# Optimization experiments

Measured on AMD Instinct MI355X. Metric: run time of the kernel, lower is better.

Reference implementation:

```python
import jax, jax.numpy as jnp
import numpy as np

D_MODEL = 512
NUM_HEADS = 8
DEPTH = D_MODEL // NUM_HEADS
B, S = 8, 1024


def setup_inputs() -> dict:
    key = jax.random.key(0)
    ks = jax.random.split(key, 14)
    scale = 1.0 / np.sqrt(D_MODEL)
    inp = {
        "q_in": jax.random.normal(ks[0], (B, S, D_MODEL), jnp.float32),
        "k_in": jax.random.normal(ks[1], (B, S, D_MODEL), jnp.float32),
        "v_in": jax.random.normal(ks[2], (B, S, D_MODEL), jnp.float32),
        # padding mask: 1 = masked-out position
        "mask": jax.random.randint(ks[3], (B, 1, 1, S), 0, 2).astype(jnp.float32),
        "additional_weights": jax.random.uniform(ks[4], (B, S, S), jnp.float32),
        "wq": jax.random.normal(ks[5], (D_MODEL, D_MODEL), jnp.float32) * scale,
        "bq": jnp.zeros((D_MODEL,), jnp.float32),
        "wk": jax.random.normal(ks[6], (D_MODEL, D_MODEL), jnp.float32) * scale,
        "bk": jnp.zeros((D_MODEL,), jnp.float32),
        "wv": jax.random.normal(ks[7], (D_MODEL, D_MODEL), jnp.float32) * scale,
        "bv": jnp.zeros((D_MODEL,), jnp.float32),
        "wo": jax.random.normal(ks[8], (D_MODEL, D_MODEL), jnp.float32) * scale,
        "bo": jnp.zeros((D_MODEL,), jnp.float32),
    }
    return inp


def _split_heads(x):
    # [B, S, d_model] -> [B, H, S, depth]
    b, s, _ = x.shape
    return x.reshape(b, s, NUM_HEADS, DEPTH).transpose(0, 2, 1, 3)


def reference(q_in, k_in, v_in, mask, additional_weights,
              wq, bq, wk, bk, wv, bv, wo, bo):
    q = _split_heads(q_in @ wq + bq)  # [B,H,S,D]
    k = _split_heads(k_in @ wk + bk)
    v = _split_heads(v_in @ wv + bv)

    scores = jnp.einsum("bhqd,bhkd->bhqk", q, k) / jnp.sqrt(
        jnp.asarray(DEPTH, q.dtype))
    scores = scores + mask * -1e9
    attn = jax.nn.softmax(scores, axis=-1)
    # post-softmax multiplicative weights, broadcast over heads
    attn = attn * additional_weights[:, None, :, :]
    x = jnp.einsum("bhqk,bhkd->bhqd", attn, v)
    x = x.transpose(0, 2, 1, 3).reshape(q_in.shape[0], -1, D_MODEL)
    out = x @ wo + bo
    return out, attn
```

## Files before the change

### kernel.cpp

```cpp
#include <hip/hip_runtime.h>
#include <stdint.h>

typedef unsigned short u16;
typedef short bf16x8 __attribute__((ext_vector_type(8)));
typedef short bf16x4 __attribute__((ext_vector_type(4)));
typedef float f32x4 __attribute__((ext_vector_type(4)));
typedef u16 u16x8 __attribute__((ext_vector_type(8)));
typedef u16 u16x4 __attribute__((ext_vector_type(4)));

#define NHEADS 8
#define SEQ 1024
#define DM 512
#define DEPTH 64
#define BATCH 8

__device__ __forceinline__ u16 f2bf(float f) {
    union { float f; unsigned u; } v; v.f = f;
    unsigned r = v.u + 0x7FFF + ((v.u >> 16) & 1);
    return (u16)(r >> 16);
}

__device__ __forceinline__ f32x4 mfma_16x16x16_bf16(bf16x4 a, bf16x4 b, f32x4 c) {
#if __has_builtin(__builtin_amdgcn_mfma_f32_16x16x16bf16_1k)
    return __builtin_amdgcn_mfma_f32_16x16x16bf16_1k(a, b, c, 0, 0, 0);
#else
    asm("v_mfma_f32_16x16x16_bf16 %0, %1, %2, %0" : "+v"(c) : "v"(a), "v"(b));
    return c;
#endif
}

__global__ void __launch_bounds__(256) transpose512(
    const float* __restrict__ w0, const float* __restrict__ w1,
    const float* __restrict__ w2, const float* __restrict__ w3,
    u16* __restrict__ wt)
{
    __shared__ float tile[32][33];
    const float* w = (blockIdx.z == 0) ? w0 : (blockIdx.z == 1) ? w1
                   : (blockIdx.z == 2) ? w2 : w3;
    u16* o = wt + (size_t)blockIdx.z * (DM * DM);
    int rb = blockIdx.y * 32, cb = blockIdx.x * 32;
    int tx = threadIdx.x, ty = threadIdx.y;
    #pragma unroll
    for (int k = 0; k < 32; k += 8)
        tile[ty + k][tx] = w[(size_t)(rb + ty + k) * DM + cb + tx];
    __syncthreads();
    #pragma unroll
    for (int k = 0; k < 32; k += 8)
        o[(size_t)(cb + ty + k) * DM + rb + tx] = f2bf(tile[tx][ty + k]);
}

__global__ void __launch_bounds__(256) conv_bf16(
    const float* __restrict__ q, const float* __restrict__ k,
    const float* __restrict__ v,
    u16* __restrict__ oq, u16* __restrict__ ok, u16* __restrict__ ov)
{
    const float* src = (blockIdx.z == 0) ? q : (blockIdx.z == 1) ? k : v;
    u16* dst = (blockIdx.z == 0) ? oq : (blockIdx.z == 1) ? ok : ov;
    size_t i = ((size_t)blockIdx.x * 256 + threadIdx.x) * 8;
    f32x4 a = *(const f32x4*)(src + i);
    f32x4 b = *(const f32x4*)(src + i + 4);
    u16x8 o;
    #pragma unroll
    for (int j = 0; j < 4; j++) { o[j] = f2bf(a[j]); o[j + 4] = f2bf(b[j]); }
    *(u16x8*)(dst + i) = o;
}

template <int LAYOUT>
__device__ __forceinline__ void gemm_tile(
    const u16* __restrict__ A, const u16* __restrict__ wt,
    const float* __restrict__ bias, void* __restrict__ out_)
{
    const int tid = threadIdx.x;
    const int wid = tid >> 6, lane = tid & 63;
    const int wm = wid >> 1, wn = wid & 1;
    const int mb = blockIdx.y * 128 + wm * 64;
    const int nb = blockIdx.x * 128 + wn * 64;
    const int lr = lane & 15, g = lane >> 4, lk = g * 8;

    f32x4 acc[4][4];
    #pragma unroll
    for (int i = 0; i < 4; i++)
        #pragma unroll
        for (int j = 0; j < 4; j++) acc[i][j] = (f32x4)0.f;

    for (int ks = 0; ks < DM; ks += 32) {
        bf16x8 a[4], bf[4];
        #pragma unroll
        for (int mt = 0; mt < 4; mt++)
            a[mt] = *(const bf16x8*)(A + (size_t)(mb + mt * 16 + lr) * DM + ks + lk);
        #pragma unroll
        for (int nt = 0; nt < 4; nt++)
            bf[nt] = *(const bf16x8*)(wt + (size_t)(nb + nt * 16 + lr) * DM + ks + lk);
        #pragma unroll
        for (int mt = 0; mt < 4; mt++)
            #pragma unroll
            for (int nt = 0; nt < 4; nt++) {
                if (LAYOUT == 1)
                    acc[mt][nt] = __builtin_amdgcn_mfma_f32_16x16x32_bf16(
                        bf[nt], a[mt], acc[mt][nt], 0, 0, 0);
                else
                    acc[mt][nt] = __builtin_amdgcn_mfma_f32_16x16x32_bf16(
                        a[mt], bf[nt], acc[mt][nt], 0, 0, 0);
            }
    }

    #pragma unroll
    for (int mt = 0; mt < 4; mt++) {
        #pragma unroll
        for (int nt = 0; nt < 4; nt++) {
            #pragma unroll
            for (int r = 0; r < 4; r++) {
                if (LAYOUT == 1) {
                    int m = mb + mt * 16 + lr;
                    int n = nb + nt * 16 + 4 * g + r;
                    float val = acc[mt][nt][r] + bias[n];
                    int b_ = m >> 10, s = m & 1023, h = n >> 6, d = n & 63;
                    ((u16*)out_)[((size_t)((b_ * NHEADS + h) << 6) + d) * SEQ + s] = f2bf(val);
                } else {
                    int n = nb + nt * 16 + lr;
                    int m = mb + mt * 16 + 4 * g + r;
                    float val = acc[mt][nt][r] + bias[n];
                    if (LAYOUT == 2) {
                        ((float*)out_)[(size_t)m * DM + n] = val;
                    } else {
                        int b_ = m >> 10, s = m & 1023, h = n >> 6, d = n & 63;
                        ((u16*)out_)[(((size_t)(b_ * NHEADS + h) * SEQ + s) << 6) + d] = f2bf(val);
                    }
                }
            }
        }
    }
}

__global__ void __launch_bounds__(256) qkv_proj(
    const u16* __restrict__ qbf, const u16* __restrict__ kbf,
    const u16* __restrict__ vbf, const u16* __restrict__ wt_base,
    const float* __restrict__ bq, const float* __restrict__ bk,
    const float* __restrict__ bv,
    u16* __restrict__ Qb, u16* __restrict__ Kb, u16* __restrict__ VTb)
{
    int z = blockIdx.z;
    if (z == 0)      gemm_tile<0>(qbf, wt_base,               bq, Qb);
    else if (z == 1) gemm_tile<0>(kbf, wt_base + DM * DM,     bk, Kb);
    else             gemm_tile<1>(vbf, wt_base + 2 * DM * DM, bv, VTb);
}

__global__ void __launch_bounds__(256) out_proj(
    const u16* __restrict__ X, const u16* __restrict__ wto,
    const float* __restrict__ bo, float* __restrict__ out)
{
    gemm_tile<2>(X, wto, bo, out);
}

__global__ void __launch_bounds__(256, 5) attn_kernel(
    const u16* __restrict__ Q, const u16* __restrict__ K,
    const u16* __restrict__ VT, const float* __restrict__ mask,
    const float* __restrict__ addw, float* __restrict__ attn_out,
    u16* __restrict__ X)
{
    __shared__ float Xr[4][16][64];
    __shared__ float redm[4][16];
    __shared__ float reds[4][16];

    const int id = blockIdx.x;
    const int c = id & 7, t = id >> 3;
    const int h = t & 7;
    const int p = ((t >> 3) << 3) | c;
    const int qt = p & 63, b = p >> 6;

    const int tid = threadIdx.x, wid = tid >> 6, lane = tid & 63;
    const int lr = lane & 15, g = lane >> 4, lk = g * 8;
    const size_t head = (size_t)(b * NHEADS + h) * (SEQ * DEPTH);
    const u16* Qh = Q + head + (size_t)qt * 16 * DEPTH;
    const u16* Kh = K + head;
    const u16* Vh = VT + head;
    const int kst = (wid << 4) + (g << 2);

    bf16x8 qf0 = *(const bf16x8*)(Qh + lr * DEPTH + lk);
    bf16x8 qf1 = *(const bf16x8*)(Qh + lr * DEPTH + 32 + lk);
    f32x4 acc[16];
    #pragma unroll
    for (int nt = 0; nt < 16; nt++) acc[nt] = (f32x4)0.f;
    #pragma unroll
    for (int nt = 0; nt < 16; nt++) {
        const u16* kp = Kh + (size_t)(nt * 64 + (wid << 4) + lr) * DEPTH + lk;
        bf16x8 k0 = *(const bf16x8*)kp;
        bf16x8 k1 = *(const bf16x8*)(kp + 32);
        acc[nt] = __builtin_amdgcn_mfma_f32_16x16x32_bf16(k0, qf0, acc[nt], 0, 0, 0);
        acc[nt] = __builtin_amdgcn_mfma_f32_16x16x32_bf16(k1, qf1, acc[nt], 0, 0, 0);
    }

    const float* mrow = mask + ((size_t)b << 10);
    float mx = -3.0e38f;
    #pragma unroll
    for (int nt = 0; nt < 16; nt++) {
        f32x4 mr = *(const f32x4*)(mrow + nt * 64 + kst);
        #pragma unroll
        for (int r = 0; r < 4; r++) {
            acc[nt][r] = acc[nt][r] * 0.125f + mr[r] * -1e9f;
            mx = fmaxf(mx, acc[nt][r]);
        }
    }
    mx = fmaxf(mx, __shfl_xor(mx, 16, 64));
    mx = fmaxf(mx, __shfl_xor(mx, 32, 64));
    if (lane < 16) redm[wid][lr] = mx;
    __syncthreads();
    float gm = fmaxf(fmaxf(redm[0][lr], redm[1][lr]),
                     fmaxf(redm[2][lr], redm[3][lr]));

    float sm = 0.f;
    #pragma unroll
    for (int nt = 0; nt < 16; nt++)
        #pragma unroll
        for (int r = 0; r < 4; r++) {
            float pv = __expf(acc[nt][r] - gm);
            acc[nt][r] = pv;
            sm += pv;
        }
    sm += __shfl_xor(sm, 16, 64);
    sm += __shfl_xor(sm, 32, 64);
    if (lane < 16) reds[wid][lr] = sm;
    __syncthreads();
    float iv = 1.0f / (reds[0][lr] + reds[1][lr] + reds[2][lr] + reds[3][lr]);

    const int qglob = (qt << 4) + lr;
    const size_t awbase = ((size_t)((b << 10) + qglob)) << 10;
    const size_t aobase = ((size_t)(((b * NHEADS + h) << 10) + qglob)) << 10;
    const u16* vb_base = Vh + (size_t)lr * SEQ;

    f32x4 x[4];
    #pragma unroll
    for (int dt = 0; dt < 4; dt++) x[dt] = (f32x4)0.f;

    #pragma unroll
    for (int nt = 0; nt < 16; nt++) {
        const int k0 = nt * 64 + kst;
        f32x4 aw = *(const f32x4*)(addw + awbase + k0);
        f32x4 o;
        bf16x4 pa;
        #pragma unroll
        for (int r = 0; r < 4; r++) {
            float v = acc[nt][r] * iv * aw[r];
            o[r] = v;
            pa[r] = (short)f2bf(v);
        }
        *(f32x4*)(attn_out + aobase + k0) = o;
        #pragma unroll
        for (int dt = 0; dt < 4; dt++) {
            bf16x4 vb = *(const bf16x4*)(vb_base + (size_t)(dt << 4) * SEQ + k0);
            x[dt] = mfma_16x16x16_bf16(pa, vb, x[dt]);
        }
    }

    #pragma unroll
    for (int dt = 0; dt < 4; dt++)
        #pragma unroll
        for (int r = 0; r < 4; r++)
            Xr[wid][4 * g + r][(dt << 4) + lr] = x[dt][r];
    __syncthreads();

    #pragma unroll
    for (int r = 0; r < 4; r++) {
        int q = 4 * g + r, d = (wid << 4) + lr;
        float s = Xr[0][q][d] + Xr[1][q][d] + Xr[2][q][d] + Xr[3][q][d];
        X[((size_t)((b << 10) + (qt << 4) + q)) * DM + (h << 6) + d] = f2bf(s);
    }
}

extern "C" void kernel_launch(void* const* d_in, const int* in_sizes, int n_in,
                              void* d_out, int out_size, void* d_ws, size_t ws_size,
                              hipStream_t stream)
{
    const float* q_in = (const float*)d_in[0];
    const float* k_in = (const float*)d_in[1];
    const float* v_in = (const float*)d_in[2];
    const float* mask = (const float*)d_in[3];
    const float* addw = (const float*)d_in[4];
    const float* wq = (const float*)d_in[5];
    const float* bq = (const float*)d_in[6];
    const float* wk = (const float*)d_in[7];
    const float* bk = (const float*)d_in[8];
    const float* wv = (const float*)d_in[9];
    const float* bv = (const float*)d_in[10];
    const float* wo = (const float*)d_in[11];
    const float* bo = (const float*)d_in[12];

    const size_t ACT = (size_t)BATCH * SEQ * DM;

    u16* ws = (u16*)d_ws;
    u16* wt  = ws;
    u16* Qb  = wt + 4 * DM * DM;
    u16* Kb  = Qb + ACT;
    u16* VTb = Kb + ACT;
    u16* Xb  = VTb + ACT;

    float* out0 = (float*)d_out;
    float* attn_out = out0 + ACT;

    u16* qbf = (u16*)attn_out;
    u16* kbf = qbf + ACT;
    u16* vbf = kbf + ACT;

    transpose512<<<dim3(16, 16, 4), dim3(32, 8), 0, stream>>>(wq, wk, wv, wo, wt);
    conv_bf16<<<dim3(2048, 1, 3), 256, 0, stream>>>(q_in, k_in, v_in, qbf, kbf, vbf);
    qkv_proj<<<dim3(4, 64, 3), 256, 0, stream>>>(qbf, kbf, vbf, wt, bq, bk, bv,
                                                 Qb, Kb, VTb);
    attn_kernel<<<dim3(4096), 256, 0, stream>>>(Qb, Kb, VTb, mask, addw,
                                                attn_out, Xb);
    out_proj<<<dim3(4, 64, 1), 256, 0, stream>>>(Xb, wt + 3 * DM * DM, bo, out0);
}
```

Baseline: 659.3 us.

## Fuse fp32-to-bf16 conversion into LDS double-buffered projection GEMMs

Drops the separate conversion kernel: the QKV projection now reads fp32 inputs directly and converts them to bf16 while staging tiles into double-buffered shared memory with padded rows. Both projection GEMMs now share A/B tiles across waves through LDS instead of each wave loading its own tiles from global memory. The attention kernel's key assignment changes so each wave handles a contiguous 256-key chunk, which alters the access pattern for K, mask, additional weights and the attention output. This removes one launch and one round trip of the activations through memory, in exchange for LDS traffic and barriers inside the GEMM loop.

Measured after the change: 602.1 us. 1.1x faster.

```diff
diff --git a/kernel.cpp b/kernel.cpp
--- a/kernel.cpp
+++ b/kernel.cpp
@@ -13,6 +13,8 @@
 #define DM 512
 #define DEPTH 64
 #define BATCH 8
+#define BK 32
+#define LDSROW 40
 
 __device__ __forceinline__ u16 f2bf(float f) {
     union { float f; unsigned u; } v; v.f = f;
@@ -49,33 +51,55 @@
         o[(size_t)(cb + ty + k) * DM + rb + tx] = f2bf(tile[tx][ty + k]);
 }
 
-__global__ void __launch_bounds__(256) conv_bf16(
-    const float* __restrict__ q, const float* __restrict__ k,
-    const float* __restrict__ v,
-    u16* __restrict__ oq, u16* __restrict__ ok, u16* __restrict__ ov)
-{
-    const float* src = (blockIdx.z == 0) ? q : (blockIdx.z == 1) ? k : v;
-    u16* dst = (blockIdx.z == 0) ? oq : (blockIdx.z == 1) ? ok : ov;
-    size_t i = ((size_t)blockIdx.x * 256 + threadIdx.x) * 8;
-    f32x4 a = *(const f32x4*)(src + i);
-    f32x4 b = *(const f32x4*)(src + i + 4);
-    u16x8 o;
-    #pragma unroll
-    for (int j = 0; j < 4; j++) { o[j] = f2bf(a[j]); o[j + 4] = f2bf(b[j]); }
-    *(u16x8*)(dst + i) = o;
-}
-
-template <int LAYOUT>
-__device__ __forceinline__ void gemm_tile(
-    const u16* __restrict__ A, const u16* __restrict__ wt,
+template <int LAYOUT, int AF32>
+__device__ __forceinline__ void gemm_tile2(
+    const void* __restrict__ Asrc, const u16* __restrict__ wt,
     const float* __restrict__ bias, void* __restrict__ out_)
 {
+    __shared__ u16 Al[2][128 * LDSROW];
+    __shared__ u16 Bl[2][128 * LDSROW];
+
     const int tid = threadIdx.x;
     const int wid = tid >> 6, lane = tid & 63;
     const int wm = wid >> 1, wn = wid & 1;
-    const int mb = blockIdx.y * 128 + wm * 64;
-    const int nb = blockIdx.x * 128 + wn * 64;
     const int lr = lane & 15, g = lane >> 4, lk = g * 8;
+    const int mb = blockIdx.y * 128;
+    const int nb = blockIdx.x * 128;
+    const int r0 = tid >> 2;
+    const int c0 = (tid & 3) * 8;
+
+    f32x4 fa0a, fa0b, fa1a, fa1b;
+    u16x8 ua0, ua1, ub0, ub1;
+
+    auto loadStage = [&](int ks) {
+        if (AF32) {
+            const float* A = (const float*)Asrc;
+            fa0a = *(const f32x4*)(A + (size_t)(mb + r0) * DM + ks + c0);
+            fa0b = *(const f32x4*)(A + (size_t)(mb + r0) * DM + ks + c0 + 4);
+            fa1a = *(const f32x4*)(A + (size_t)(mb + 64 + r0) * DM + ks + c0);
+            fa1b = *(const f32x4*)(A + (size_t)(mb + 64 + r0) * DM + ks + c0 + 4);
+        } else {
+            const u16* A = (const u16*)Asrc;
+            ua0 = *(const u16x8*)(A + (size_t)(mb + r0) * DM + ks + c0);
+            ua1 = *(const u16x8*)(A + (size_t)(mb + 64 + r0) * DM + ks + c0);
+        }
+        ub0 = *(const u16x8*)(wt + (size_t)(nb + r0) * DM + ks + c0);
+        ub1 = *(const u16x8*)(wt + (size_t)(nb + 64 + r0) * DM + ks + c0);
+    };
+    auto writeStage = [&](int buf) {
+        u16x8 w0, w1;
+        if (AF32) {
+            #pragma unroll
+            for (int j = 0; j < 4; j++) {
+                w0[j] = f2bf(fa0a[j]); w0[j + 4] = f2bf(fa0b[j]);
+                w1[j] = f2bf(fa1a[j]); w1[j + 4] = f2bf(fa1b[j]);
+            }
+        } else { w0 = ua0; w1 = ua1; }
+        *(u16x8*)(&Al[buf][r0 * LDSROW + c0]) = w0;
+        *(u16x8*)(&Al[buf][(64 + r0) * LDSROW + c0]) = w1;
+        *(u16x8*)(&Bl[buf][r0 * LDSROW + c0]) = ub0;
+        *(u16x8*)(&Bl[buf][(64 + r0) * LDSROW + c0]) = ub1;
+    };
 
     f32x4 acc[4][4];
     #pragma unroll
@@ -83,24 +107,30 @@
         #pragma unroll
         for (int j = 0; j < 4; j++) acc[i][j] = (f32x4)0.f;
 
-    for (int ks = 0; ks < DM; ks += 32) {
-        bf16x8 a[4], bf[4];
+    loadStage(0);
+    for (int ks = 0, step = 0; ks < DM; ks += BK, step++) {
+        const int buf = step & 1;
+        writeStage(buf);
+        if (ks + BK < DM) loadStage(ks + BK);
+        __syncthreads();
+
+        bf16x8 af[4], bf4[4];
         #pragma unroll
         for (int mt = 0; mt < 4; mt++)
-            a[mt] = *(const bf16x8*)(A + (size_t)(mb + mt * 16 + lr) * DM + ks + lk);
+            af[mt] = *(const bf16x8*)(&Al[buf][(wm * 64 + mt * 16 + lr) * LDSROW + lk]);
         #pragma unroll
         for (int nt = 0; nt < 4; nt++)
-            bf[nt] = *(const bf16x8*)(wt + (size_t)(nb + nt * 16 + lr) * DM + ks + lk);
+            bf4[nt] = *(const bf16x8*)(&Bl[buf][(wn * 64 + nt * 16 + lr) * LDSROW + lk]);
         #pragma unroll
         for (int mt = 0; mt < 4; mt++)
             #pragma unroll
             for (int nt = 0; nt < 4; nt++) {
                 if (LAYOUT == 1)
                     acc[mt][nt] = __builtin_amdgcn_mfma_f32_16x16x32_bf16(
-                        bf[nt], a[mt], acc[mt][nt], 0, 0, 0);
+                        bf4[nt], af[mt], acc[mt][nt], 0, 0, 0);
                 else
                     acc[mt][nt] = __builtin_amdgcn_mfma_f32_16x16x32_bf16(
-                        a[mt], bf[nt], acc[mt][nt], 0, 0, 0);
+                        af[mt], bf4[nt], acc[mt][nt], 0, 0, 0);
             }
     }
 
@@ -111,14 +141,14 @@
             #pragma unroll
             for (int r = 0; r < 4; r++) {
                 if (LAYOUT == 1) {
-                    int m = mb + mt * 16 + lr;
-                    int n = nb + nt * 16 + 4 * g + r;
+                    int m = mb + wm * 64 + mt * 16 + lr;
+                    int n = nb + wn * 64 + nt * 16 + 4 * g + r;
                     float val = acc[mt][nt][r] + bias[n];
                     int b_ = m >> 10, s = m & 1023, h = n >> 6, d = n & 63;
                     ((u16*)out_)[((size_t)((b_ * NHEADS + h) << 6) + d) * SEQ + s] = f2bf(val);
                 } else {
-                    int n = nb + nt * 16 + lr;
-                    int m = mb + mt * 16 + 4 * g + r;
+                    int n = nb + wn * 64 + nt * 16 + lr;
+                    int m = mb + wm * 64 + mt * 16 + 4 * g + r;
                     float val = acc[mt][nt][r] + bias[n];
                     if (LAYOUT == 2) {
                         ((float*)out_)[(size_t)m * DM + n] = val;
@@ -133,23 +163,23 @@
 }
 
 __global__ void __launch_bounds__(256) qkv_proj(
-    const u16* __restrict__ qbf, const u16* __restrict__ kbf,
-    const u16* __restrict__ vbf, const u16* __restrict__ wt_base,
+    const float* __restrict__ q_in, const float* __restrict__ k_in,
+    const float* __restrict__ v_in, const u16* __restrict__ wt_base,
     const float* __restrict__ bq, const float* __restrict__ bk,
     const float* __restrict__ bv,
     u16* __restrict__ Qb, u16* __restrict__ Kb, u16* __restrict__ VTb)
 {
     int z = blockIdx.z;
-    if (z == 0)      gemm_tile<0>(qbf, wt_base,               bq, Qb);
-    else if (z == 1) gemm_tile<0>(kbf, wt_base + DM * DM,     bk, Kb);
-    else             gemm_tile<1>(vbf, wt_base + 2 * DM * DM, bv, VTb);
+    if (z == 0)      gemm_tile2<0, 1>(q_in, wt_base,              bq, Qb);
+    else if (z == 1) gemm_tile2<0, 1>(k_in, wt_base + DM * DM,    bk, Kb);
+    else             gemm_tile2<1, 1>(v_in, wt_base + 2 * DM * DM, bv, VTb);
 }
 
 __global__ void __launch_bounds__(256) out_proj(
     const u16* __restrict__ X, const u16* __restrict__ wto,
     const float* __restrict__ bo, float* __restrict__ out)
 {
-    gemm_tile<2>(X, wto, bo, out);
+    gemm_tile2<2, 0>(X, wto, bo, out);
 }
 
 __global__ void __launch_bounds__(256, 5) attn_kernel(
@@ -174,7 +204,7 @@
     const u16* Qh = Q + head + (size_t)qt * 16 * DEPTH;
     const u16* Kh = K + head;
     const u16* Vh = VT + head;
-    const int kst = (wid << 4) + (g << 2);
+    const int wbase = wid << 8;
 
     bf16x8 qf0 = *(const bf16x8*)(Qh + lr * DEPTH + lk);
     bf16x8 qf1 = *(const bf16x8*)(Qh + lr * DEPTH + 32 + lk);
@@ -183,7 +213,7 @@
     for (int nt = 0; nt < 16; nt++) acc[nt] = (f32x4)0.f;
     #pragma unroll
     for (int nt = 0; nt < 16; nt++) {
-        const u16* kp = Kh + (size_t)(nt * 64 + (wid << 4) + lr) * DEPTH + lk;
+        const u16* kp = Kh + (size_t)(wbase + (nt << 4) + lr) * DEPTH + lk;
         bf16x8 k0 = *(const bf16x8*)kp;
         bf16x8 k1 = *(const bf16x8*)(kp + 32);
         acc[nt] = __builtin_amdgcn_mfma_f32_16x16x32_bf16(k0, qf0, acc[nt], 0, 0, 0);
@@ -194,7 +224,7 @@
     float mx = -3.0e38f;
     #pragma unroll
     for (int nt = 0; nt < 16; nt++) {
-        f32x4 mr = *(const f32x4*)(mrow + nt * 64 + kst);
+        f32x4 mr = *(const f32x4*)(mrow + wbase + (nt << 4) + 4 * g);
         #pragma unroll
         for (int r = 0; r < 4; r++) {
             acc[nt][r] = acc[nt][r] * 0.125f + mr[r] * -1e9f;
@@ -234,8 +264,8 @@
 
     #pragma unroll
     for (int nt = 0; nt < 16; nt++) {
-        const int k0 = nt * 64 + kst;
-        f32x4 aw = *(const f32x4*)(addw + awbase + k0);
+        const int kk = wbase + (nt << 4) + 4 * g;
+        f32x4 aw = *(const f32x4*)(addw + awbase + kk);
         f32x4 o;
         bf16x4 pa;
         #pragma unroll
@@ -244,10 +274,10 @@
             o[r] = v;
             pa[r] = (short)f2bf(v);
         }
-        *(f32x4*)(attn_out + aobase + k0) = o;
+        *(f32x4*)(attn_out + aobase + kk) = o;
         #pragma unroll
         for (int dt = 0; dt < 4; dt++) {
-            bf16x4 vb = *(const bf16x4*)(vb_base + (size_t)(dt << 4) * SEQ + k0);
+            bf16x4 vb = *(const bf16x4*)(vb_base + (size_t)(dt << 4) * SEQ + kk);
             x[dt] = mfma_16x16x16_bf16(pa, vb, x[dt]);
         }
     }
@@ -297,14 +327,9 @@
     float* out0 = (float*)d_out;
     float* attn_out = out0 + ACT;
 
-    u16* qbf = (u16*)attn_out;
-    u16* kbf = qbf + ACT;
-    u16* vbf = kbf + ACT;
-
     transpose512<<<dim3(16, 16, 4), dim3(32, 8), 0, stream>>>(wq, wk, wv, wo, wt);
-    conv_bf16<<<dim3(2048, 1, 3), 256, 0, stream>>>(q_in, k_in, v_in, qbf, kbf, vbf);
-    qkv_proj<<<dim3(4, 64, 3), 256, 0, stream>>>(qbf, kbf, vbf, wt, bq, bk, bv,
-                                                 Qb, Kb, VTb);
+    qkv_proj<<<dim3(4, 64, 3), 256, 0, stream>>>(q_in, k_in, v_in, wt,
+                                                 bq, bk, bv, Qb, Kb, VTb);
     attn_kernel<<<dim3(4096), 256, 0, stream>>>(Qb, Kb, VTb, mask, addw,
                                                 attn_out, Xb);
     out_proj<<<dim3(4, 64, 1), 256, 0, stream>>>(Xb, wt + 3 * DM * DM, bo, out0);
```
